# Optimization experiments

Measured on AMD Instinct MI355X. Metric: run time of the kernel, lower is better.

Reference implementation:

```python
import jax, jax.numpy as jnp
import numpy as np

SPARSITY = 0.01

def quantize(weight, s):
    # ternary quantization: (-s, 0, +s); computed under no_grad in torch
    pos = (weight > s).astype(weight.dtype)
    neg = (weight < -s).astype(weight.dtype)
    return (pos - neg) * s

def setup_inputs() -> dict:
    key = jax.random.key(0)
    k1, k2, k3 = jax.random.split(key, 3)
    B, N, Din, Dout = 8, 2048, 256, 256
    x = jax.random.normal(k1, (B, N, Din), dtype=jnp.float32)
    adj = jax.random.uniform(k2, (B, N, N), dtype=jnp.float32)
    # xavier_uniform_ over (in_dim, out_dim)
    limit = float(np.sqrt(6.0 / (Din + Dout)))
    weight = jax.random.uniform(k3, (Din, Dout), dtype=jnp.float32, minval=-limit, maxval=limit)
    bias = jnp.zeros((Dout,), dtype=jnp.float32)
    return {"x": x, "adj": adj, "weight": weight, "bias": bias}

def reference(x, adj, weight, bias):
    dw = quantize(weight, SPARSITY)          # [Din, Dout] ternary * s
    support = jnp.einsum('bni,io->bno', x, dw)   # [B, N, Dout]
    out = jnp.einsum('bnm,bmo->bno', adj, support) + bias
    return jax.nn.relu(out)
```

## Files before the change

### kernel.cpp

```cpp
#include <hip/hip_runtime.h>
#include <stdint.h>

typedef __attribute__((ext_vector_type(8))) short short8;
typedef __attribute__((ext_vector_type(4))) float f32x4;

static_assert(sizeof(short8) == 16, "frag size");

__device__ __forceinline__ uint16_t f2bf(float f) {
  uint32_t u = __builtin_bit_cast(uint32_t, f);
  u += 0x7fffu + ((u >> 16) & 1u);
  return (uint16_t)(u >> 16);
}

__device__ __forceinline__ void gload_lds16(const void* g, void* lds_wave_base) {
  __builtin_amdgcn_global_load_lds(
      (__attribute__((address_space(1))) void*)(void*)(g),
      (__attribute__((address_space(3))) void*)(lds_wave_base),
      16, 0, 0);
}


__global__ __launch_bounds__(256) void quant_kernel(const float* __restrict__ w,
                                                    uint16_t* __restrict__ dwT) {
  const int o = blockIdx.x, i = threadIdx.x;
  const float v = w[i * 256 + o];
  const float t = (v > 0.01f) ? 1.0f : ((v < -0.01f) ? -1.0f : 0.0f);
  dwT[o * 256 + (i ^ ((o & 7) << 3))] = f2bf(t);
}

#define SB_A 0
#define SB_B 32768

__global__ __launch_bounds__(256) void support_kernel(const float* __restrict__ x,
                                                      const uint16_t* __restrict__ dwT,
                                                      uint16_t* __restrict__ spt) {
  __shared__ __align__(16) unsigned char smem[65536];
  const int t = threadIdx.x, lane = t & 63, w = t >> 6;
  const int r = lane & 15, q = lane >> 4;
  const int g0 = (blockIdx.x & 255) * 64;
  const int o0 = (blockIdx.x >> 8) * 64;

#pragma unroll
  for (int j = 0; j < 8; ++j) {
    const int id = j * 256 + t;
    const int row = id >> 5, c = id & 31;
    const float* p = x + (size_t)(g0 + row) * 256 + c * 8;
    const f32x4 v0 = *(const f32x4*)p;
    const f32x4 v1 = *(const f32x4*)(p + 4);
    uint4 u;
    u.x = (uint32_t)f2bf(v0.x) | ((uint32_t)f2bf(v0.y) << 16);
    u.y = (uint32_t)f2bf(v0.z) | ((uint32_t)f2bf(v0.w) << 16);
    u.z = (uint32_t)f2bf(v1.x) | ((uint32_t)f2bf(v1.y) << 16);
    u.w = (uint32_t)f2bf(v1.z) | ((uint32_t)f2bf(v1.w) << 16);
    *(uint4*)(smem + SB_A + row * 512 + ((c ^ (row & 7)) << 4)) = u;
  }
#pragma unroll
  for (int j = 0; j < 8; ++j) {
    const int id = j * 256 + t, row = id >> 5, c = id & 31;
    gload_lds16(dwT + (size_t)(o0 + row) * 256 + c * 8,
                smem + SB_B + (size_t)(j * 256 + w * 64) * 16);
  }
  __syncthreads();

  f32x4 acc[4] = {};
#pragma unroll
  for (int h = 0; h < 8; ++h) {
    short8 av, bv[4];
    const int pc = (((h * 4 + q) ^ (r & 7)) << 4);
    av = *(const short8*)(smem + SB_A + (16 * w + r) * 512 + pc);
#pragma unroll
    for (int ni = 0; ni < 4; ++ni)
      bv[ni] = *(const short8*)(smem + SB_B + (16 * ni + r) * 512 + pc);
#pragma unroll
    for (int ni = 0; ni < 4; ++ni)
      acc[ni] = __builtin_amdgcn_mfma_f32_16x16x32_bf16(av, bv[ni], acc[ni], 0, 0, 0);
  }
  __syncthreads();

#pragma unroll
  for (int ni = 0; ni < 4; ++ni) {
    const int ol = 16 * ni + r;
#pragma unroll
    for (int reg = 0; reg < 4; ++reg) {
      const int gl = 16 * w + 4 * q + reg;
      const int gsw = gl ^ ((ol & 7) << 3);
      *(uint16_t*)(smem + (ol * 64 + gsw) * 2) = f2bf(acc[ni][reg] * 0.01f);
    }
  }
  __syncthreads();
#pragma unroll
  for (int it = 0; it < 2; ++it) {
    const int id = it * 256 + t, row = id >> 3, cc = id & 7;
    const uint4 u = *(const uint4*)(smem + (row * 64 + cc * 8) * 2);
    *(uint4*)(spt + (size_t)(o0 + row) * 16384 + g0 + cc * 8) = u;
  }
}

#define MB_A 0
#define MB_B 8192

__global__ __launch_bounds__(256) void gcn_main_kernel(const float* __restrict__ adj,
                                                       const uint16_t* __restrict__ spt,
                                                       const float* __restrict__ bias,
                                                       float* __restrict__ out) {
  __shared__ __align__(16) unsigned char smem[73728];
  const int t = threadIdx.x, lane = t & 63, w = t >> 6;
  const int r = lane & 15, q = lane >> 4;
  const int bb = blockIdx.x & 7;
  const int n0 = (blockIdx.x >> 3) * 32;
  const float* adjb = adj + ((size_t)bb * 2048 + n0) * 2048;
  const uint16_t* sptb = spt + (size_t)bb * 2048;

  f32x4 acc[2][4] = {};

  for (int k0 = 0; k0 < 2048; k0 += 128) {
#pragma unroll
    for (int it = 0; it < 2; ++it) {
      const int id = it * 256 + t;
      const int row = id >> 4, c = id & 15;
      const float* p = adjb + (size_t)row * 2048 + k0 + c * 8;
      const f32x4 v0 = *(const f32x4*)p;
      const f32x4 v1 = *(const f32x4*)(p + 4);
      uint4 u;
      u.x = (uint32_t)f2bf(v0.x) | ((uint32_t)f2bf(v0.y) << 16);
      u.y = (uint32_t)f2bf(v0.z) | ((uint32_t)f2bf(v0.w) << 16);
      u.z = (uint32_t)f2bf(v1.x) | ((uint32_t)f2bf(v1.y) << 16);
      u.w = (uint32_t)f2bf(v1.z) | ((uint32_t)f2bf(v1.w) << 16);
      *(uint4*)(smem + MB_A + row * 256 + ((c ^ (row & 7)) << 4)) = u;
    }
#pragma unroll
    for (int j = 0; j < 16; ++j) {
      const int id = j * 256 + t, row = id >> 4, c = id & 15;
      gload_lds16(sptb + (size_t)row * 16384 + k0 + c * 8,
                  smem + MB_B + (size_t)(j * 256 + w * 64) * 16);
    }
    __syncthreads();
#pragma unroll
    for (int h = 0; h < 4; ++h) {
      short8 av[2], bv[4];
      const int pc = (((h * 4 + q) ^ (r & 7)) << 4);
#pragma unroll
      for (int mi = 0; mi < 2; ++mi)
        av[mi] = *(const short8*)(smem + MB_A + (16 * mi + r) * 256 + pc);
#pragma unroll
      for (int ni = 0; ni < 4; ++ni)
        bv[ni] = *(const short8*)(smem + MB_B + (w * 64 + 16 * ni + r) * 256 + pc);
#pragma unroll
      for (int mi = 0; mi < 2; ++mi)
#pragma unroll
        for (int ni = 0; ni < 4; ++ni)
          acc[mi][ni] = __builtin_amdgcn_mfma_f32_16x16x32_bf16(av[mi], bv[ni],
                                                                acc[mi][ni], 0, 0, 0);
    }
    __syncthreads();
  }
#pragma unroll
  for (int ni = 0; ni < 4; ++ni) {
    const int o = w * 64 + 16 * ni + r;
    const float bs = bias[o];
#pragma unroll
    for (int mi = 0; mi < 2; ++mi)
#pragma unroll
      for (int reg = 0; reg < 4; ++reg) {
        const int n = n0 + 16 * mi + 4 * q + reg;
        out[((size_t)bb * 2048 + n) * 256 + o] = fmaxf(acc[mi][ni][reg] + bs, 0.0f);
      }
  }
}

extern "C" void kernel_launch(void* const* d_in, const int* in_sizes, int n_in,
                              void* d_out, int out_size, void* d_ws, size_t ws_size,
                              hipStream_t stream) {
  const float* x      = (const float*)d_in[0];
  const float* adj    = (const float*)d_in[1];
  const float* weight = (const float*)d_in[2];
  const float* bias   = (const float*)d_in[3];
  float* out = (float*)d_out;

  uint16_t* dwT = (uint16_t*)d_ws;
  uint16_t* spt = (uint16_t*)((char*)d_ws + 131072);

  hipLaunchKernelGGL(quant_kernel,    dim3(256),  dim3(256), 0, stream, weight, dwT);
  hipLaunchKernelGGL(support_kernel,  dim3(1024), dim3(256), 0, stream, x, dwT, spt);
  hipLaunchKernelGGL(gcn_main_kernel, dim3(512),  dim3(256), 0, stream, adj, spt, bias, out);
}
```

Measured before the change: 230.1 us.

## Double-buffer adj and support tiles in GCN main kernel with K=64 steps

Reworks the main aggregation loop into a two-stage software pipeline. The next tile's adj values are loaded into registers and the support tile is fetched asynchronously into an alternate LDS buffer while MFMAs run on the current tile. The K step is halved to 64 so the double buffers fit in LDS, and only one barrier is used per iteration. This is meant to hide global-load latency behind compute, at the cost of more iterations and more live registers.

```diff
diff --git a/kernel.cpp b/kernel.cpp
--- a/kernel.cpp
+++ b/kernel.cpp
@@ -96,8 +96,10 @@
   }
 }
 
-#define MB_A 0
-#define MB_B 8192
+#define MB_A0 0
+#define MB_A1 4096
+#define MB_B0 8192
+#define MB_B1 40960
 
 __global__ __launch_bounds__(256) void gcn_main_kernel(const float* __restrict__ adj,
                                                        const uint16_t* __restrict__ spt,
@@ -111,49 +113,79 @@
   const float* adjb = adj + ((size_t)bb * 2048 + n0) * 2048;
   const uint16_t* sptb = spt + (size_t)bb * 2048;
 
+  const int aRow = t >> 3, aC = t & 7;
+  const float* aP = adjb + (size_t)aRow * 2048 + aC * 8;
+  const unsigned aOff = aRow * 128 + ((aC ^ (aRow & 7)) << 4);
+
+  {
+    const f32x4 v0 = *(const f32x4*)(aP);
+    const f32x4 v1 = *(const f32x4*)(aP + 4);
+#pragma unroll
+    for (int j = 0; j < 8; ++j) {
+      const int id = j * 256 + t, row = id >> 3, c = id & 7;
+      gload_lds16(sptb + (size_t)row * 16384 + c * 8,
+                  smem + MB_B0 + (size_t)(j * 256 + w * 64) * 16);
+    }
+    uint4 u;
+    u.x = (uint32_t)f2bf(v0.x) | ((uint32_t)f2bf(v0.y) << 16);
+    u.y = (uint32_t)f2bf(v0.z) | ((uint32_t)f2bf(v0.w) << 16);
+    u.z = (uint32_t)f2bf(v1.x) | ((uint32_t)f2bf(v1.y) << 16);
+    u.w = (uint32_t)f2bf(v1.z) | ((uint32_t)f2bf(v1.w) << 16);
+    *(uint4*)(smem + MB_A0 + aOff) = u;
+  }
+  __syncthreads();
+
   f32x4 acc[2][4] = {};
-
-  for (int k0 = 0; k0 < 2048; k0 += 128) {
-#pragma unroll
-    for (int it = 0; it < 2; ++it) {
-      const int id = it * 256 + t;
-      const int row = id >> 4, c = id & 15;
-      const float* p = adjb + (size_t)row * 2048 + k0 + c * 8;
-      const f32x4 v0 = *(const f32x4*)p;
-      const f32x4 v1 = *(const f32x4*)(p + 4);
+  for (int kt = 0; kt < 32; ++kt) {
+    const int cur = kt & 1;
+    const unsigned aCur = cur ? MB_A1 : MB_A0;
+    const unsigned bCur = cur ? MB_B1 : MB_B0;
+    const unsigned aNxt = cur ? MB_A0 : MB_A1;
+    const unsigned bNxt = cur ? MB_B0 : MB_B1;
+    const int k1 = (kt + 1) * 64;
+    const bool pf = (kt < 31);
+
+    f32x4 v0, v1;
+    if (pf) {
+      v0 = *(const f32x4*)(aP + k1);
+      v1 = *(const f32x4*)(aP + k1 + 4);
+#pragma unroll
+      for (int j = 0; j < 8; ++j) {
+        const int id = j * 256 + t, row = id >> 3, c = id & 7;
+        gload_lds16(sptb + (size_t)row * 16384 + k1 + c * 8,
+                    smem + bNxt + (size_t)(j * 256 + w * 64) * 16);
+      }
+    }
+
+#pragma unroll
+    for (int h = 0; h < 2; ++h) {
+      short8 av[2], bv[4];
+      const int pc = (((h * 4 + q) ^ (r & 7)) << 4);
+#pragma unroll
+      for (int mi = 0; mi < 2; ++mi)
+        av[mi] = *(const short8*)(smem + aCur + (16 * mi + r) * 128 + pc);
+#pragma unroll
+      for (int ni = 0; ni < 4; ++ni)
+        bv[ni] = *(const short8*)(smem + bCur + (w * 64 + 16 * ni + r) * 128 + pc);
+#pragma unroll
+      for (int mi = 0; mi < 2; ++mi)
+#pragma unroll
+        for (int ni = 0; ni < 4; ++ni)
+          acc[mi][ni] = __builtin_amdgcn_mfma_f32_16x16x32_bf16(av[mi], bv[ni],
+                                                                acc[mi][ni], 0, 0, 0);
+    }
+
+    if (pf) {
       uint4 u;
       u.x = (uint32_t)f2bf(v0.x) | ((uint32_t)f2bf(v0.y) << 16);
       u.y = (uint32_t)f2bf(v0.z) | ((uint32_t)f2bf(v0.w) << 16);
       u.z = (uint32_t)f2bf(v1.x) | ((uint32_t)f2bf(v1.y) << 16);
       u.w = (uint32_t)f2bf(v1.z) | ((uint32_t)f2bf(v1.w) << 16);
-      *(uint4*)(smem + MB_A + row * 256 + ((c ^ (row & 7)) << 4)) = u;
-    }
-#pragma unroll
-    for (int j = 0; j < 16; ++j) {
-      const int id = j * 256 + t, row = id >> 4, c = id & 15;
-      gload_lds16(sptb + (size_t)row * 16384 + k0 + c * 8,
-                  smem + MB_B + (size_t)(j * 256 + w * 64) * 16);
+      *(uint4*)(smem + aNxt + aOff) = u;
     }
     __syncthreads();
-#pragma unroll
-    for (int h = 0; h < 4; ++h) {
-      short8 av[2], bv[4];
-      const int pc = (((h * 4 + q) ^ (r & 7)) << 4);
-#pragma unroll
-      for (int mi = 0; mi < 2; ++mi)
-        av[mi] = *(const short8*)(smem + MB_A + (16 * mi + r) * 256 + pc);
-#pragma unroll
-      for (int ni = 0; ni < 4; ++ni)
-        bv[ni] = *(const short8*)(smem + MB_B + (w * 64 + 16 * ni + r) * 256 + pc);
-#pragma unroll
-      for (int mi = 0; mi < 2; ++mi)
-#pragma unroll
-        for (int ni = 0; ni < 4; ++ni)
-          acc[mi][ni] = __builtin_amdgcn_mfma_f32_16x16x32_bf16(av[mi], bv[ni],
-                                                                acc[mi][ni], 0, 0, 0);
-    }
-    __syncthreads();
-  }
+  }
+
 #pragma unroll
   for (int ni = 0; ni < 4; ++ni) {
     const int o = w * 64 + 16 * ni + r;
```

After: 237.4 us. 3.2% more time.

## Double-buffer main GEMM K-loop with register prefetch of adj and async B DMA

Applied to the files above, without the earlier changes.

Restructures the main adj×support kernel into a K=64 step loop with double-buffered LDS for both the adj tile and the support tile. Support tiles for the next step are issued as async global-to-LDS loads, and adj values are prefetched two steps ahead into registers. Manual s_waitcnt and s_barrier calls replace the two __syncthreads per iteration so memory latency can overlap the MFMA work. This raises LDS use to 80KB, which may cut occupancy, and the hand-counted vmcnt waits are fragile if the compiler reorders memory operations.

```diff
diff --git a/kernel.cpp b/kernel.cpp
--- a/kernel.cpp
+++ b/kernel.cpp
@@ -18,6 +18,8 @@
       (__attribute__((address_space(3))) void*)(lds_wave_base),
       16, 0, 0);
 }
+
+#define MEMFENCE() asm volatile("" ::: "memory")
 
 
 __global__ __launch_bounds__(256) void quant_kernel(const float* __restrict__ w,
@@ -96,14 +98,16 @@
   }
 }
 
-#define MB_A 0
-#define MB_B 8192
+#define MB_A0 0
+#define MB_A1 8192
+#define MB_B0 16384
+#define MB_B1 81920
 
 __global__ __launch_bounds__(256) void gcn_main_kernel(const float* __restrict__ adj,
                                                        const uint16_t* __restrict__ spt,
                                                        const float* __restrict__ bias,
                                                        float* __restrict__ out) {
-  __shared__ __align__(16) unsigned char smem[73728];
+  __shared__ __align__(16) unsigned char smem[81920];
   const int t = threadIdx.x, lane = t & 63, w = t >> 6;
   const int r = lane & 15, q = lane >> 4;
   const int bb = blockIdx.x & 7;
@@ -111,40 +115,108 @@
   const float* adjb = adj + ((size_t)bb * 2048 + n0) * 2048;
   const uint16_t* sptb = spt + (size_t)bb * 2048;
 
+  const int aRow = t >> 4, aC = t & 15;
+  const float* aP0 = adjb + (size_t)aRow * 2048 + aC * 8;
+  const float* aP1 = aP0 + (size_t)16 * 2048;
+  const unsigned aOff0 = aRow * 256 + ((aC ^ (aRow & 7)) << 4);
+  const unsigned aOff1 = aOff0 + 16 * 256;
+
+#define MB_BH0 16384u
+#define MB_BH1 49152u
+
+#define B_DMA(K0, BOFF)                                                        \
+  do {                                                                         \
+    _Pragma("unroll") for (int j = 0; j < 8; ++j) {                            \
+      const int id = j * 256 + t, row_ = id >> 3, c_ = id & 7;                 \
+      gload_lds16(sptb + (size_t)row_ * 16384 + (K0) + c_ * 8,                 \
+                  smem + (BOFF) + (size_t)(j * 256 + w * 64) * 16);            \
+    }                                                                          \
+  } while (0)
+
+#define A_LOAD(K0, R0, R1, S0, S1)                                             \
+  do {                                                                         \
+    R0 = *(const f32x4*)(aP0 + (K0));                                          \
+    S0 = *(const f32x4*)(aP0 + (K0) + 4);                                      \
+    R1 = *(const f32x4*)(aP1 + (K0));                                          \
+    S1 = *(const f32x4*)(aP1 + (K0) + 4);                                      \
+  } while (0)
+
+#define A_WRITE(AOFF, R0, S0, R1, S1)                                          \
+  do {                                                                         \
+    uint4 u0, u1;                                                              \
+    u0.x = (uint32_t)f2bf(R0.x) | ((uint32_t)f2bf(R0.y) << 16);                \
+    u0.y = (uint32_t)f2bf(R0.z) | ((uint32_t)f2bf(R0.w) << 16);                \
+    u0.z = (uint32_t)f2bf(S0.x) | ((uint32_t)f2bf(S0.y) << 16);                \
+    u0.w = (uint32_t)f2bf(S0.z) | ((uint32_t)f2bf(S0.w) << 16);                \
+    u1.x = (uint32_t)f2bf(R1.x) | ((uint32_t)f2bf(R1.y) << 16);                \
+    u1.y = (uint32_t)f2bf(R1.z) | ((uint32_t)f2bf(R1.w) << 16);                \
+    u1.z = (uint32_t)f2bf(S1.x) | ((uint32_t)f2bf(S1.y) << 16);                \
+    u1.w = (uint32_t)f2bf(S1.z) | ((uint32_t)f2bf(S1.w) << 16);                \
+    *(uint4*)(smem + (AOFF) + aOff0) = u0;                                     \
+    *(uint4*)(smem + (AOFF) + aOff1) = u1;                                     \
+  } while (0)
+
+#undef A_LOAD
+#undef A_WRITE
+  const int a64Row = t >> 3, a64C = t & 7;
+  const float* a64P = adjb + (size_t)a64Row * 2048 + a64C * 8;
+  const unsigned a64Off = a64Row * 128 + ((a64C ^ (a64Row & 7)) << 4);
+#define MB_AH0 0u
+#define MB_AH1 4096u
+
   f32x4 acc[2][4] = {};
 
-  for (int k0 = 0; k0 < 2048; k0 += 128) {
-#pragma unroll
-    for (int it = 0; it < 2; ++it) {
-      const int id = it * 256 + t;
-      const int row = id >> 4, c = id & 15;
-      const float* p = adjb + (size_t)row * 2048 + k0 + c * 8;
-      const f32x4 v0 = *(const f32x4*)p;
-      const f32x4 v1 = *(const f32x4*)(p + 4);
-      uint4 u;
-      u.x = (uint32_t)f2bf(v0.x) | ((uint32_t)f2bf(v0.y) << 16);
-      u.y = (uint32_t)f2bf(v0.z) | ((uint32_t)f2bf(v0.w) << 16);
-      u.z = (uint32_t)f2bf(v1.x) | ((uint32_t)f2bf(v1.y) << 16);
-      u.w = (uint32_t)f2bf(v1.z) | ((uint32_t)f2bf(v1.w) << 16);
-      *(uint4*)(smem + MB_A + row * 256 + ((c ^ (row & 7)) << 4)) = u;
-    }
-#pragma unroll
-    for (int j = 0; j < 16; ++j) {
-      const int id = j * 256 + t, row = id >> 4, c = id & 15;
-      gload_lds16(sptb + (size_t)row * 16384 + k0 + c * 8,
-                  smem + MB_B + (size_t)(j * 256 + w * 64) * 16);
-    }
-    __syncthreads();
-#pragma unroll
-    for (int h = 0; h < 4; ++h) {
+  MEMFENCE();
+  B_DMA(0, MB_BH0);
+  MEMFENCE();
+  f32x4 p0 = *(const f32x4*)(a64P);
+  f32x4 p1 = *(const f32x4*)(a64P + 4);
+  MEMFENCE();
+  f32x4 n0v = *(const f32x4*)(a64P + 64);
+  f32x4 n1v = *(const f32x4*)(a64P + 68);
+  MEMFENCE();
+  {
+    uint4 u;
+    u.x = (uint32_t)f2bf(p0.x) | ((uint32_t)f2bf(p0.y) << 16);
+    u.y = (uint32_t)f2bf(p0.z) | ((uint32_t)f2bf(p0.w) << 16);
+    u.z = (uint32_t)f2bf(p1.x) | ((uint32_t)f2bf(p1.y) << 16);
+    u.w = (uint32_t)f2bf(p1.z) | ((uint32_t)f2bf(p1.w) << 16);
+    *(uint4*)(smem + MB_AH0 + a64Off) = u;
+  }
+  asm volatile("s_waitcnt vmcnt(2) lgkmcnt(0)" ::: "memory");
+  __builtin_amdgcn_s_barrier();
+  p0 = n0v; p1 = n1v;
+
+  for (int kt = 0; kt < 32; ++kt) {
+    const int cur = kt & 1;
+    const unsigned aCur = cur ? MB_AH1 : MB_AH0;
+    const unsigned bCur = cur ? MB_BH1 : MB_BH0;
+    const unsigned aNxt = cur ? MB_AH0 : MB_AH1;
+    const unsigned bNxt = cur ? MB_BH0 : MB_BH1;
+    const int k1 = (kt + 1) * 64;
+
+    if (kt < 31) {
+      MEMFENCE();
+      B_DMA(k1, bNxt);
+      MEMFENCE();
+    }
+    f32x4 q0, q1;
+    if (kt < 30) {
+      q0 = *(const f32x4*)(a64P + (kt + 2) * 64);
+      q1 = *(const f32x4*)(a64P + (kt + 2) * 64 + 4);
+      MEMFENCE();
+    }
+
+#pragma unroll
+    for (int h = 0; h < 2; ++h) {
       short8 av[2], bv[4];
       const int pc = (((h * 4 + q) ^ (r & 7)) << 4);
 #pragma unroll
       for (int mi = 0; mi < 2; ++mi)
-        av[mi] = *(const short8*)(smem + MB_A + (16 * mi + r) * 256 + pc);
+        av[mi] = *(const short8*)(smem + aCur + (16 * mi + r) * 128 + pc);
 #pragma unroll
       for (int ni = 0; ni < 4; ++ni)
-        bv[ni] = *(const short8*)(smem + MB_B + (w * 64 + 16 * ni + r) * 256 + pc);
+        bv[ni] = *(const short8*)(smem + bCur + (w * 64 + 16 * ni + r) * 128 + pc);
 #pragma unroll
       for (int mi = 0; mi < 2; ++mi)
 #pragma unroll
@@ -152,8 +224,24 @@
           acc[mi][ni] = __builtin_amdgcn_mfma_f32_16x16x32_bf16(av[mi], bv[ni],
                                                                 acc[mi][ni], 0, 0, 0);
     }
-    __syncthreads();
-  }
+
+    if (kt < 31) {
+      uint4 u;
+      u.x = (uint32_t)f2bf(p0.x) | ((uint32_t)f2bf(p0.y) << 16);
+      u.y = (uint32_t)f2bf(p0.z) | ((uint32_t)f2bf(p0.w) << 16);
+      u.z = (uint32_t)f2bf(p1.x) | ((uint32_t)f2bf(p1.y) << 16);
+      u.w = (uint32_t)f2bf(p1.z) | ((uint32_t)f2bf(p1.w) << 16);
+      *(uint4*)(smem + aNxt + a64Off) = u;
+      if (kt < 30) {
+        asm volatile("s_waitcnt vmcnt(2) lgkmcnt(0)" ::: "memory");
+      } else {
+        asm volatile("s_waitcnt vmcnt(0) lgkmcnt(0)" ::: "memory");
+      }
+      __builtin_amdgcn_s_barrier();
+      p0 = q0; p1 = q1;
+    }
+  }
+
 #pragma unroll
   for (int ni = 0; ni < 4; ++ni) {
     const int o = w * 64 + 16 * ni + r;
```

Result: slower. 237.6 us (+3.2%).

## Load MFMA fragments directly from global with register double-buffering, drop LDS

Applied to the files above, without the earlier changes.

The main GCN kernel no longer stages adj and support tiles through shared memory. Each lane now loads its MFMA A and B fragments straight from global memory, converts adj to bf16 in registers, and ping-pongs two register sets so the next k-slice loads while the current one computes. This removes the LDS round trips and block-wide barriers, and adds a `__launch_bounds__(256, 3)` occupancy hint. The cost is less coalesced global access and no on-chip sharing of fragments across waves, so reuse now depends on the caches. The support kernel's store path also now undoes the LDS swizzle on read, so the support tensor comes out in the intended order.

```diff
diff --git a/kernel.cpp b/kernel.cpp
--- a/kernel.cpp
+++ b/kernel.cpp
@@ -12,13 +12,21 @@
   return (uint16_t)(u >> 16);
 }
 
+__device__ __forceinline__ short8 pack_bf16x8(f32x4 lo, f32x4 hi) {
+  union { uint32_t u[4]; short8 s; } z;
+  z.u[0] = (uint32_t)f2bf(lo.x) | ((uint32_t)f2bf(lo.y) << 16);
+  z.u[1] = (uint32_t)f2bf(lo.z) | ((uint32_t)f2bf(lo.w) << 16);
+  z.u[2] = (uint32_t)f2bf(hi.x) | ((uint32_t)f2bf(hi.y) << 16);
+  z.u[3] = (uint32_t)f2bf(hi.z) | ((uint32_t)f2bf(hi.w) << 16);
+  return z.s;
+}
+
 __device__ __forceinline__ void gload_lds16(const void* g, void* lds_wave_base) {
   __builtin_amdgcn_global_load_lds(
       (__attribute__((address_space(1))) void*)(void*)(g),
       (__attribute__((address_space(3))) void*)(lds_wave_base),
       16, 0, 0);
 }
-
 
 __global__ __launch_bounds__(256) void quant_kernel(const float* __restrict__ w,
                                                     uint16_t* __restrict__ dwT) {
@@ -91,72 +99,75 @@
 #pragma unroll
   for (int it = 0; it < 2; ++it) {
     const int id = it * 256 + t, row = id >> 3, cc = id & 7;
-    const uint4 u = *(const uint4*)(smem + (row * 64 + cc * 8) * 2);
+    const uint4 u = *(const uint4*)(smem + (row * 64 + ((cc ^ (row & 7)) * 8)) * 2);
     *(uint4*)(spt + (size_t)(o0 + row) * 16384 + g0 + cc * 8) = u;
   }
 }
 
-#define MB_A 0
-#define MB_B 8192
-
-__global__ __launch_bounds__(256) void gcn_main_kernel(const float* __restrict__ adj,
-                                                       const uint16_t* __restrict__ spt,
-                                                       const float* __restrict__ bias,
-                                                       float* __restrict__ out) {
-  __shared__ __align__(16) unsigned char smem[73728];
+__global__ __launch_bounds__(256, 3) void gcn_main_kernel(const float* __restrict__ adj,
+                                                          const uint16_t* __restrict__ spt,
+                                                          const float* __restrict__ bias,
+                                                          float* __restrict__ out) {
   const int t = threadIdx.x, lane = t & 63, w = t >> 6;
   const int r = lane & 15, q = lane >> 4;
   const int bb = blockIdx.x & 7;
   const int n0 = (blockIdx.x >> 3) * 32;
+  const int ob = w * 64;
   const float* adjb = adj + ((size_t)bb * 2048 + n0) * 2048;
   const uint16_t* sptb = spt + (size_t)bb * 2048;
 
+  const float* aR0 = adjb + (size_t)r * 2048 + q * 8;
+  const float* aR1 = adjb + (size_t)(r + 16) * 2048 + q * 8;
+  const uint16_t* bR0 = sptb + (size_t)(ob + r) * 16384 + q * 8;
+  const uint16_t* bR1 = bR0 + (size_t)16 * 16384;
+  const uint16_t* bR2 = bR0 + (size_t)32 * 16384;
+  const uint16_t* bR3 = bR0 + (size_t)48 * 16384;
+
   f32x4 acc[2][4] = {};
 
-  for (int k0 = 0; k0 < 2048; k0 += 128) {
-#pragma unroll
-    for (int it = 0; it < 2; ++it) {
-      const int id = it * 256 + t;
-      const int row = id >> 4, c = id & 15;
-      const float* p = adjb + (size_t)row * 2048 + k0 + c * 8;
-      const f32x4 v0 = *(const f32x4*)p;
-      const f32x4 v1 = *(const f32x4*)(p + 4);
-      uint4 u;
-      u.x = (uint32_t)f2bf(v0.x) | ((uint32_t)f2bf(v0.y) << 16);
-      u.y = (uint32_t)f2bf(v0.z) | ((uint32_t)f2bf(v0.w) << 16);
-      u.z = (uint32_t)f2bf(v1.x) | ((uint32_t)f2bf(v1.y) << 16);
-      u.w = (uint32_t)f2bf(v1.z) | ((uint32_t)f2bf(v1.w) << 16);
-      *(uint4*)(smem + MB_A + row * 256 + ((c ^ (row & 7)) << 4)) = u;
-    }
-#pragma unroll
-    for (int j = 0; j < 16; ++j) {
-      const int id = j * 256 + t, row = id >> 4, c = id & 15;
-      gload_lds16(sptb + (size_t)row * 16384 + k0 + c * 8,
-                  smem + MB_B + (size_t)(j * 256 + w * 64) * 16);
-    }
-    __syncthreads();
-#pragma unroll
-    for (int h = 0; h < 4; ++h) {
-      short8 av[2], bv[4];
-      const int pc = (((h * 4 + q) ^ (r & 7)) << 4);
-#pragma unroll
-      for (int mi = 0; mi < 2; ++mi)
-        av[mi] = *(const short8*)(smem + MB_A + (16 * mi + r) * 256 + pc);
-#pragma unroll
-      for (int ni = 0; ni < 4; ++ni)
-        bv[ni] = *(const short8*)(smem + MB_B + (w * 64 + 16 * ni + r) * 256 + pc);
-#pragma unroll
-      for (int mi = 0; mi < 2; ++mi)
-#pragma unroll
-        for (int ni = 0; ni < 4; ++ni)
-          acc[mi][ni] = __builtin_amdgcn_mfma_f32_16x16x32_bf16(av[mi], bv[ni],
-                                                                acc[mi][ni], 0, 0, 0);
-    }
-    __syncthreads();
+#define LOAD_SET(A0, A1, A2, A3, B0, B1, B2, B3, KO)                           \
+  do {                                                                         \
+    A0 = *(const f32x4*)(aR0 + (KO));                                          \
+    A1 = *(const f32x4*)(aR0 + (KO) + 4);                                      \
+    A2 = *(const f32x4*)(aR1 + (KO));                                          \
+    A3 = *(const f32x4*)(aR1 + (KO) + 4);                                      \
+    B0 = *(const short8*)(bR0 + (KO));                                         \
+    B1 = *(const short8*)(bR1 + (KO));                                         \
+    B2 = *(const short8*)(bR2 + (KO));                                         \
+    B3 = *(const short8*)(bR3 + (KO));                                         \
+  } while (0)
+
+#define COMPUTE_SET(A0, A1, A2, A3, B0, B1, B2, B3)                            \
+  do {                                                                         \
+    const short8 av0 = pack_bf16x8(A0, A1);                                    \
+    const short8 av1 = pack_bf16x8(A2, A3);                                    \
+    acc[0][0] = __builtin_amdgcn_mfma_f32_16x16x32_bf16(av0, B0, acc[0][0], 0, 0, 0); \
+    acc[0][1] = __builtin_amdgcn_mfma_f32_16x16x32_bf16(av0, B1, acc[0][1], 0, 0, 0); \
+    acc[0][2] = __builtin_amdgcn_mfma_f32_16x16x32_bf16(av0, B2, acc[0][2], 0, 0, 0); \
+    acc[0][3] = __builtin_amdgcn_mfma_f32_16x16x32_bf16(av0, B3, acc[0][3], 0, 0, 0); \
+    acc[1][0] = __builtin_amdgcn_mfma_f32_16x16x32_bf16(av1, B0, acc[1][0], 0, 0, 0); \
+    acc[1][1] = __builtin_amdgcn_mfma_f32_16x16x32_bf16(av1, B1, acc[1][1], 0, 0, 0); \
+    acc[1][2] = __builtin_amdgcn_mfma_f32_16x16x32_bf16(av1, B2, acc[1][2], 0, 0, 0); \
+    acc[1][3] = __builtin_amdgcn_mfma_f32_16x16x32_bf16(av1, B3, acc[1][3], 0, 0, 0); \
+  } while (0)
+
+  f32x4 xa0, xa1, xa2, xa3; short8 xb0, xb1, xb2, xb3;
+  f32x4 ya0, ya1, ya2, ya3; short8 yb0, yb1, yb2, yb3;
+  LOAD_SET(xa0, xa1, xa2, xa3, xb0, xb1, xb2, xb3, 0);
+  LOAD_SET(ya0, ya1, ya2, ya3, yb0, yb1, yb2, yb3, 32);
+
+  for (int kt = 0; kt < 2048; kt += 64) {
+    COMPUTE_SET(xa0, xa1, xa2, xa3, xb0, xb1, xb2, xb3);
+    if (kt + 64 < 2048)
+      LOAD_SET(xa0, xa1, xa2, xa3, xb0, xb1, xb2, xb3, kt + 64);
+    COMPUTE_SET(ya0, ya1, ya2, ya3, yb0, yb1, yb2, yb3);
+    if (kt + 96 < 2048)
+      LOAD_SET(ya0, ya1, ya2, ya3, yb0, yb1, yb2, yb3, kt + 96);
   }
+
 #pragma unroll
   for (int ni = 0; ni < 4; ++ni) {
-    const int o = w * 64 + 16 * ni + r;
+    const int o = ob + 16 * ni + r;
     const float bs = bias[o];
 #pragma unroll
     for (int mi = 0; mi < 2; ++mi)
@@ -166,6 +177,8 @@
         out[((size_t)bb * 2048 + n) * 256 + o] = fmaxf(acc[mi][ni][reg] + bs, 0.0f);
       }
   }
+#undef LOAD_SET
+#undef COMPUTE_SET
 }
 
 extern "C" void kernel_launch(void* const* d_in, const int* in_sizes, int n_in,
```

New measurement: 305.7 us. +32.8%, slower.
